# Kernel tuning notes

Hardware: AMD Instinct MI355X
Metric: run time of the kernel (lower is better)

Reference implementation:

```python
import jax, jax.numpy as jnp
import numpy as np

# SMPL 24-joint kinematic tree (parent of joint j); root has parent -1.
PARENTS = [-1, 0, 0, 0, 1, 2, 3, 4, 5, 6, 7, 8, 9, 9, 9, 12, 13, 14, 16, 17, 18, 19, 20, 21]
N_JOINTS = len(PARENTS)  # 24


def setup_inputs() -> dict:
    key = jax.random.key(0)
    k1, k2 = jax.random.split(key)
    N = 262144
    joint_angles = jax.random.normal(k1, (N, N_JOINTS * 9), dtype=jnp.float32)
    offsets = jax.random.normal(k2, (N_JOINTS, 3), dtype=jnp.float32)
    return {"joint_angles": joint_angles, "offsets": offsets}


def reference(joint_angles, offsets):
    # joint_angles: (N, n_joints*9) -> (N, n_joints, 3, 3)
    N = joint_angles.shape[0]
    ang = joint_angles.reshape(N, N_JOINTS, 3, 3)
    # no_root=True: force the root rotation to identity
    ang = ang.at[:, 0].set(jnp.eye(3, dtype=ang.dtype))

    rotations = [ang[:, 0]]                              # (N,3,3)
    positions = [jnp.zeros((N, 3), dtype=ang.dtype)]     # (N,3)
    # Sequential tree recurrence over fixed small joint count (right-mult path,
    # left_mult=False): pos_j = R_parent @ offset_j + pos_parent;
    # R_j = R_parent @ A_j.
    for j in range(1, N_JOINTS):
        p = PARENTS[j]
        pos = jnp.einsum('nij,j->ni', rotations[p], offsets[j]) + positions[p]
        rot = jnp.einsum('nij,njk->nik', rotations[p], ang[:, j])
        positions.append(pos)
        rotations.append(rot)

    return jnp.stack(positions, axis=1)  # (N, n_joints, 3)
```

## Files before the change

kernel.cpp:

```cpp
#include <hip/hip_runtime.h>

namespace {

typedef float v4f __attribute__((ext_vector_type(4)));

struct M3 { float a[9]; };
struct V3 { float x, y, z; };

__device__ __forceinline__ V3 mulv_add(const M3& R, V3 o, V3 p) {
    V3 r;
    r.x = fmaf(R.a[0], o.x, fmaf(R.a[1], o.y, fmaf(R.a[2], o.z, p.x)));
    r.y = fmaf(R.a[3], o.x, fmaf(R.a[4], o.y, fmaf(R.a[5], o.z, p.y)));
    r.z = fmaf(R.a[6], o.x, fmaf(R.a[7], o.y, fmaf(R.a[8], o.z, p.z)));
    return r;
}

__device__ __forceinline__ M3 mulm(const M3& R, const M3& A) {
    M3 D;
#pragma unroll
    for (int i = 0; i < 3; ++i) {
#pragma unroll
        for (int k = 0; k < 3; ++k) {
            D.a[i*3+k] = fmaf(R.a[i*3+0], A.a[0*3+k],
                         fmaf(R.a[i*3+1], A.a[1*3+k],
                              R.a[i*3+2] * A.a[2*3+k]));
        }
    }
    return D;
}

template <int REL>
__device__ __forceinline__ float getf(const float4* s) {
    constexpr int Q = REL >> 2;
    constexpr int C = REL & 3;
    if constexpr (C == 0) return s[Q].x;
    else if constexpr (C == 1) return s[Q].y;
    else if constexpr (C == 2) return s[Q].z;
    else return s[Q].w;
}

template <int J, int BASE>
__device__ __forceinline__ M3 loadA(const float4* s) {
    constexpr int K = 9 * J - BASE;
    M3 A;
    A.a[0] = getf<K+0>(s); A.a[1] = getf<K+1>(s); A.a[2] = getf<K+2>(s);
    A.a[3] = getf<K+3>(s); A.a[4] = getf<K+4>(s); A.a[5] = getf<K+5>(s);
    A.a[6] = getf<K+6>(s); A.a[7] = getf<K+7>(s); A.a[8] = getf<K+8>(s);
    return A;
}

__device__ __forceinline__ V3 loadOff(const float* __restrict__ off, int j) {
    V3 o; o.x = off[3*j+0]; o.y = off[3*j+1]; o.z = off[3*j+2]; return o;
}

#define OBP(J, P) do { ob[3*(J)+0] = (P).x; ob[3*(J)+1] = (P).y; ob[3*(J)+2] = (P).z; } while (0)

__global__ __launch_bounds__(128, 2)
void fk_kernel(const float* __restrict__ ja, const float* __restrict__ off,
               float* __restrict__ out, int N) {
    __shared__ __align__(16) float4 stage[2][18][65];

    const int t = threadIdx.x;
    const int w = t >> 6, l = t & 63;
    const int n = blockIdx.x * 128 + t;

    const float4* v4 = reinterpret_cast<const float4*>(ja) + (size_t)n * 54;

    float4 s1[21];
#pragma unroll
    for (int q = 0; q < 21; ++q) s1[q] = v4[2 + q];
    float4 s2[7];
#pragma unroll
    for (int q = 0; q < 7; ++q) s2[q] = v4[27 + q];
    float4 s3[14];
#pragma unroll
    for (int q = 0; q < 14; ++q) s3[q] = v4[36 + q];

    constexpr int B1 = 8, B2 = 108, B3 = 144;

    float ob[72];
    ob[0] = 0.f; ob[1] = 0.f; ob[2] = 0.f;

    V3 p1 = loadOff(off, 1), p2 = loadOff(off, 2), p3 = loadOff(off, 3);
    OBP(1, p1); OBP(2, p2); OBP(3, p3);
    M3 R1 = loadA<1, B1>(s1);
    M3 R2 = loadA<2, B1>(s1);
    M3 R3 = loadA<3, B1>(s1);

    V3 p4 = mulv_add(R1, loadOff(off, 4), p1);  M3 R4 = mulm(R1, loadA<4, B1>(s1));  OBP(4, p4);
    V3 p5 = mulv_add(R2, loadOff(off, 5), p2);  M3 R5 = mulm(R2, loadA<5, B1>(s1));  OBP(5, p5);
    V3 p6 = mulv_add(R3, loadOff(off, 6), p3);  M3 R6 = mulm(R3, loadA<6, B1>(s1));  OBP(6, p6);
    V3 p7 = mulv_add(R4, loadOff(off, 7), p4);  M3 R7 = mulm(R4, loadA<7, B1>(s1));  OBP(7, p7);
    V3 p8 = mulv_add(R5, loadOff(off, 8), p5);  M3 R8 = mulm(R5, loadA<8, B1>(s1));  OBP(8, p8);
    V3 p9 = mulv_add(R6, loadOff(off, 9), p6);  M3 R9 = mulm(R6, loadA<9, B1>(s1));  OBP(9, p9);

    V3 p10 = mulv_add(R7, loadOff(off, 10), p7);  OBP(10, p10);
    V3 p11 = mulv_add(R8, loadOff(off, 11), p8);  OBP(11, p11);

    V3 p12 = mulv_add(R9, loadOff(off, 12), p9);  M3 R12 = mulm(R9, loadA<12, B2>(s2));  OBP(12, p12);
    V3 p13 = mulv_add(R9, loadOff(off, 13), p9);  M3 R13 = mulm(R9, loadA<13, B2>(s2));  OBP(13, p13);
    V3 p14 = mulv_add(R9, loadOff(off, 14), p9);  M3 R14 = mulm(R9, loadA<14, B2>(s2));  OBP(14, p14);
    V3 p15 = mulv_add(R12, loadOff(off, 15), p12);  OBP(15, p15);

    V3 p16 = mulv_add(R13, loadOff(off, 16), p13);  M3 R16 = mulm(R13, loadA<16, B3>(s3));  OBP(16, p16);
    V3 p17 = mulv_add(R14, loadOff(off, 17), p14);  M3 R17 = mulm(R14, loadA<17, B3>(s3));  OBP(17, p17);
    V3 p18 = mulv_add(R16, loadOff(off, 18), p16);  M3 R18 = mulm(R16, loadA<18, B3>(s3));  OBP(18, p18);
    V3 p19 = mulv_add(R17, loadOff(off, 19), p17);  M3 R19 = mulm(R17, loadA<19, B3>(s3));  OBP(19, p19);
    V3 p20 = mulv_add(R18, loadOff(off, 20), p18);  M3 R20 = mulm(R18, loadA<20, B3>(s3));  OBP(20, p20);
    V3 p21 = mulv_add(R19, loadOff(off, 21), p19);  M3 R21 = mulm(R19, loadA<21, B3>(s3));  OBP(21, p21);

    V3 p22 = mulv_add(R20, loadOff(off, 22), p20);  OBP(22, p22);
    V3 p23 = mulv_add(R21, loadOff(off, 23), p21);  OBP(23, p23);

#pragma unroll
    for (int r = 0; r < 18; ++r) {
        float4 v;
        v.x = ob[4*r+0]; v.y = ob[4*r+1]; v.z = ob[4*r+2]; v.w = ob[4*r+3];
        stage[w][r][l] = v;
    }

    v4f* o4 = reinterpret_cast<v4f*>(out);
    const size_t base4 = ((size_t)blockIdx.x * 128 + w * 64) * 18;
#pragma unroll
    for (int i = 0; i < 18; ++i) {
        int e4 = i * 64 + l;
        int s  = e4 / 18;
        int r  = e4 - s * 18;
        float4 v = stage[w][r][s];
        v4f vv; vv.x = v.x; vv.y = v.y; vv.z = v.z; vv.w = v.w;
        __builtin_nontemporal_store(vv, &o4[base4 + e4]);
    }
}

}

extern "C" void kernel_launch(void* const* d_in, const int* in_sizes, int n_in,
                              void* d_out, int out_size, void* d_ws, size_t ws_size,
                              hipStream_t stream) {
    const float* ja  = (const float*)d_in[0];
    const float* off = (const float*)d_in[1];
    float* out = (float*)d_out;

    int N = in_sizes[0] / 216;
    int block = 128;
    int grid = (N + block - 1) / block;
    hipLaunchKernelGGL(fk_kernel, dim3(grid), dim3(block), 0, stream, ja, off, out, N);
}
```

Measured before the change: 53.81 us.

## Stage input rows via coalesced global_load_lds with staged waitcnt pipelining

Replaces the per-thread strided float4 loads of each sample's 216-float row with wave-cooperative global-to-LDS direct loads that are coalesced across the block, then reads each thread's rows back from LDS. The loads are issued in three groups, with partial vmcnt waits so computation on the first joints overlaps the arrival of later data. The block shrinks to one 64-thread wave, which uses a 43KB LDS buffer that is reused for output staging. Risks include no stage-1 barrier, relying on single-wave ordering of LDS writes from global_load_lds, LDS bank conflicts on stride-21/7/14 reads, lower occupancy from the large LDS footprint, and no tail handling when N is not divisible by 64.

```diff
diff --git a/kernel.cpp b/kernel.cpp
--- a/kernel.cpp
+++ b/kernel.cpp
@@ -53,33 +53,58 @@
     V3 o; o.x = off[3*j+0]; o.y = off[3*j+1]; o.z = off[3*j+2]; return o;
 }
 
+__device__ __forceinline__ void gload16(const float4* src, float4* lds_base) {
+    __builtin_amdgcn_global_load_lds(
+        (const __attribute__((address_space(1))) void*)src,
+        (__attribute__((address_space(3))) void*)lds_base, 16, 0, 0);
+}
+
 #define OBP(J, P) do { ob[3*(J)+0] = (P).x; ob[3*(J)+1] = (P).y; ob[3*(J)+2] = (P).z; } while (0)
 
-__global__ __launch_bounds__(128, 2)
+__global__ __launch_bounds__(64)
 void fk_kernel(const float* __restrict__ ja, const float* __restrict__ off,
-               float* __restrict__ out, int N) {
-    __shared__ __align__(16) float4 stage[2][18][65];
+               float* __restrict__ out) {
+    __shared__ __align__(16) float4 lds[2688];
+    float4* A1 = lds;
+    float4* A2 = lds + 1344;
+    float4* A3 = lds + 1792;
+    float4* stage = lds;
 
-    const int t = threadIdx.x;
-    const int w = t >> 6, l = t & 63;
-    const int n = blockIdx.x * 128 + t;
+    const int l = threadIdx.x;
+    const size_t blockBase = (size_t)blockIdx.x * 64;
+    const float4* g = reinterpret_cast<const float4*>(ja) + blockBase * 54;
 
-    const float4* v4 = reinterpret_cast<const float4*>(ja) + (size_t)n * 54;
-
-    float4 s1[21];
 #pragma unroll
-    for (int q = 0; q < 21; ++q) s1[q] = v4[2 + q];
-    float4 s2[7];
+    for (int k = 0; k < 21; ++k) {
+        int p = k * 64 + l;
+        int s = p / 21, j = p - s * 21;
+        gload16(g + s * 54 + 2 + j, A1 + k * 64);
+    }
 #pragma unroll
-    for (int q = 0; q < 7; ++q) s2[q] = v4[27 + q];
-    float4 s3[14];
+    for (int k = 0; k < 7; ++k) {
+        int p = k * 64 + l;
+        int s = p / 7, j = p - s * 7;
+        gload16(g + s * 54 + 27 + j, A2 + k * 64);
+    }
 #pragma unroll
-    for (int q = 0; q < 14; ++q) s3[q] = v4[36 + q];
-
-    constexpr int B1 = 8, B2 = 108, B3 = 144;
+    for (int k = 0; k < 14; ++k) {
+        int p = k * 64 + l;
+        int s = p / 14, j = p - s * 14;
+        gload16(g + s * 54 + 36 + j, A3 + k * 64);
+    }
 
     float ob[72];
     ob[0] = 0.f; ob[1] = 0.f; ob[2] = 0.f;
+
+    asm volatile("s_waitcnt vmcnt(21)" ::: "memory");
+
+    float4 s1[21];
+    {
+        const float4* r1 = A1 + l * 21;
+#pragma unroll
+        for (int c = 0; c < 21; ++c) s1[c] = r1[c];
+    }
+    constexpr int B1 = 8, B2 = 108, B3 = 144;
 
     V3 p1 = loadOff(off, 1), p2 = loadOff(off, 2), p3 = loadOff(off, 3);
     OBP(1, p1); OBP(2, p2); OBP(3, p3);
@@ -97,10 +122,26 @@
     V3 p10 = mulv_add(R7, loadOff(off, 10), p7);  OBP(10, p10);
     V3 p11 = mulv_add(R8, loadOff(off, 11), p8);  OBP(11, p11);
 
+    asm volatile("s_waitcnt vmcnt(14)" ::: "memory");
+    float4 s2[7];
+    {
+        const float4* r2 = A2 + l * 7;
+#pragma unroll
+        for (int c = 0; c < 7; ++c) s2[c] = r2[c];
+    }
+
     V3 p12 = mulv_add(R9, loadOff(off, 12), p9);  M3 R12 = mulm(R9, loadA<12, B2>(s2));  OBP(12, p12);
     V3 p13 = mulv_add(R9, loadOff(off, 13), p9);  M3 R13 = mulm(R9, loadA<13, B2>(s2));  OBP(13, p13);
     V3 p14 = mulv_add(R9, loadOff(off, 14), p9);  M3 R14 = mulm(R9, loadA<14, B2>(s2));  OBP(14, p14);
     V3 p15 = mulv_add(R12, loadOff(off, 15), p12);  OBP(15, p15);
+
+    asm volatile("s_waitcnt vmcnt(0)" ::: "memory");
+    float4 s3[14];
+    {
+        const float4* r3 = A3 + l * 14;
+#pragma unroll
+        for (int c = 0; c < 14; ++c) s3[c] = r3[c];
+    }
 
     V3 p16 = mulv_add(R13, loadOff(off, 16), p13);  M3 R16 = mulm(R13, loadA<16, B3>(s3));  OBP(16, p16);
     V3 p17 = mulv_add(R14, loadOff(off, 17), p14);  M3 R17 = mulm(R14, loadA<17, B3>(s3));  OBP(17, p17);
@@ -112,21 +153,22 @@
     V3 p22 = mulv_add(R20, loadOff(off, 22), p20);  OBP(22, p22);
     V3 p23 = mulv_add(R21, loadOff(off, 23), p21);  OBP(23, p23);
 
+    asm volatile("" ::: "memory");
 #pragma unroll
     for (int r = 0; r < 18; ++r) {
         float4 v;
         v.x = ob[4*r+0]; v.y = ob[4*r+1]; v.z = ob[4*r+2]; v.w = ob[4*r+3];
-        stage[w][r][l] = v;
+        stage[r * 65 + l] = v;
     }
 
     v4f* o4 = reinterpret_cast<v4f*>(out);
-    const size_t base4 = ((size_t)blockIdx.x * 128 + w * 64) * 18;
+    const size_t base4 = blockBase * 18;
 #pragma unroll
     for (int i = 0; i < 18; ++i) {
         int e4 = i * 64 + l;
         int s  = e4 / 18;
         int r  = e4 - s * 18;
-        float4 v = stage[w][r][s];
+        float4 v = stage[r * 65 + s];
         v4f vv; vv.x = v.x; vv.y = v.y; vv.z = v.z; vv.w = v.w;
         __builtin_nontemporal_store(vv, &o4[base4 + e4]);
     }
@@ -142,7 +184,6 @@
     float* out = (float*)d_out;
 
     int N = in_sizes[0] / 216;
-    int block = 128;
-    int grid = (N + block - 1) / block;
-    hipLaunchKernelGGL(fk_kernel, dim3(grid), dim3(block), 0, stream, ja, off, out, N);
+    int grid = N / 64;
+    hipLaunchKernelGGL(fk_kernel, dim3(grid), dim3(64), 0, stream, ja, off, out);
 }
```

Measured after the change: 54.04 us. Within noise of the previous version (+0.4%).
